# Kernel tuning notes

Hardware: AMD Instinct MI355X
Metric: run time of the kernel (lower is better)

Reference implementation:

```python
import jax, jax.numpy as jnp
import numpy as np

N_NODES = 100000
N_EDGES = 500000
N_REL = 6
IN_DIM = 64
HID = 128
HEADS = 4
C = HID // HEADS  # 32 per-head channels
N_GRAPHS = 1024
EPS = 1e-16


def setup_inputs() -> dict:
    key = jax.random.key(0)
    ks = jax.random.split(key, 20)
    x = jax.random.normal(ks[0], (N_NODES, IN_DIM), dtype=jnp.float32)
    edge_index = jax.random.randint(ks[1], (N_REL, 2, N_EDGES), 0, N_NODES, dtype=jnp.int64)
    batch = jnp.sort(jax.random.randint(ks[2], (N_NODES,), 0, N_GRAPHS, dtype=jnp.int64))
    s = 0.02
    return {
        "x": x, "edge_index": edge_index, "batch": batch,
        # layer1 GAT params (stacked over 6 relations)
        "W1": jax.random.normal(ks[3], (N_REL, IN_DIM, HID), dtype=jnp.float32) * s,
        "as1": jax.random.normal(ks[4], (N_REL, HEADS, C), dtype=jnp.float32) * s,
        "ad1": jax.random.normal(ks[5], (N_REL, HEADS, C), dtype=jnp.float32) * s,
        "b1": jnp.zeros((N_REL, HID), dtype=jnp.float32),
        # layer2 GAT params
        "W2": jax.random.normal(ks[6], (N_REL, HID, HID), dtype=jnp.float32) * s,
        "as2": jax.random.normal(ks[7], (N_REL, HEADS, C), dtype=jnp.float32) * s,
        "ad2": jax.random.normal(ks[8], (N_REL, HEADS, C), dtype=jnp.float32) * s,
        "b2": jnp.zeros((N_REL, HID), dtype=jnp.float32),
        # layernorms
        "g1": jnp.ones((HID,), dtype=jnp.float32), "be1": jnp.zeros((HID,), dtype=jnp.float32),
        "g2": jnp.ones((HID,), dtype=jnp.float32), "be2": jnp.zeros((HID,), dtype=jnp.float32),
        # attention pooling query + output proj
        "q": jax.random.normal(ks[9], (HID,), dtype=jnp.float32) * s,
        "Wp": jax.random.normal(ks[10], (HID, HID), dtype=jnp.float32) * s,
        "bp": jnp.zeros((HID,), dtype=jnp.float32),
    }


def _gat_hetero_layer(x, edge_index, W, a_src, a_dst, b):
    # HeteroConv(aggr='sum') over R GATConv relations, add_self_loops=False, eval (no dropout)
    N = x.shape[0]
    out = jnp.zeros((N, HEADS * C), dtype=x.dtype)
    for r in range(N_REL):
        h = (x @ W[r]).reshape(N, HEADS, C)          # [N,H,C]
        al_s = (h * a_src[r]).sum(-1)                # [N,H]
        al_d = (h * a_dst[r]).sum(-1)                # [N,H]
        src, dst = edge_index[r, 0], edge_index[r, 1]
        e = jax.nn.leaky_relu(al_s[src] + al_d[dst], 0.2)   # [E,H]
        m = jax.ops.segment_max(e, dst, num_segments=N)
        ex = jnp.exp(e - m[dst])
        den = jax.ops.segment_sum(ex, dst, num_segments=N)
        alpha = ex / (den[dst] + EPS)                # segment softmax over incoming edges
        msg = h[src] * alpha[:, :, None]             # [E,H,C]
        agg = jax.ops.segment_sum(msg, dst, num_segments=N).reshape(N, HEADS * C)
        out = out + agg + b[r]
    return out


def _layernorm(x, g, b):
    mu = x.mean(-1, keepdims=True)
    v = ((x - mu) ** 2).mean(-1, keepdims=True)
    return (x - mu) * jax.lax.rsqrt(v + 1e-5) * g + b


def _softsign(x):
    return x / (1.0 + jnp.abs(x))


def reference(x, edge_index, batch, W1, as1, ad1, b1, W2, as2, ad2, b2,
              g1, be1, g2, be2, q, Wp, bp):
    h = _gat_hetero_layer(x, edge_index, W1, as1, ad1, b1)
    h = _layernorm(_softsign(h), g1, be1)
    h = _gat_hetero_layer(h, edge_index, W2, as2, ad2, b2)
    h = _layernorm(_softsign(h), g2, be2)
    # attention pooling: segment softmax over batch, then weighted scatter-sum
    scores = (h * q).sum(-1)                                   # [N]
    m = jax.ops.segment_max(scores, batch, num_segments=N_GRAPHS)
    ex = jnp.exp(scores - m[batch])
    den = jax.ops.segment_sum(ex, batch, num_segments=N_GRAPHS)
    w = ex / (den[batch] + EPS)
    pooled = jax.ops.segment_sum(h * w[:, None], batch, num_segments=N_GRAPHS)  # [G,HID]
    return pooled @ Wp + bp
```

## Files before the change

### kernel.cpp

```cpp
#include <hip/hip_runtime.h>
#include <hip/hip_bf16.h>
#include <hip/hip_fp16.h>

#define N_NODES_C 100000
#define N_EDGES_C 500000
#define N_REL_C 6
#define IN_DIM_C 64
#define HID_C 128
#define HEADS_C 4
#define CPH_C 32
#define N_GRAPHS_C 1024
#define NBLK_SCAN 391

typedef _Float16 f16x8 __attribute__((ext_vector_type(8)));
typedef float f32x4 __attribute__((ext_vector_type(4)));

__global__ __launch_bounds__(256) void hist_rank_kernel(const int* __restrict__ ei,
                                                        int* __restrict__ cnt,
                                                        int* __restrict__ rank) {
    int i = blockIdx.x * 256 + threadIdx.x;
    if (i >= N_REL_C * N_EDGES_C) return;
    int r = i / N_EDGES_C;
    int e = i - r * N_EDGES_C;
    int dst = ei[(size_t)r * 2 * N_EDGES_C + N_EDGES_C + e];
    rank[i] = atomicAdd(&cnt[r * N_NODES_C + dst], 1);
}

__global__ __launch_bounds__(256) void scan1_kernel(const int* __restrict__ cnt,
                                                    int* __restrict__ rowptr,
                                                    int* __restrict__ blocksums) {
    int r = blockIdx.y, b = blockIdx.x, t = threadIdx.x;
    int idx = b * 256 + t;
    int v = (idx < N_NODES_C) ? cnt[r * N_NODES_C + idx] : 0;
    int orig = v;
    int lane = t & 63, w = t >> 6;
#pragma unroll
    for (int off = 1; off < 64; off <<= 1) {
        int n = __shfl_up(v, off);
        if (lane >= off) v += n;
    }
    __shared__ int wt[4];
    if (lane == 63) wt[w] = v;
    __syncthreads();
    int add = 0;
    for (int i = 0; i < w; i++) add += wt[i];
    v += add;
    if (idx < N_NODES_C) rowptr[(size_t)r * (N_NODES_C + 1) + idx] = v - orig;
    if (t == 255) blocksums[r * NBLK_SCAN + b] = v;
}

__global__ __launch_bounds__(512) void scan2_kernel(int* __restrict__ blocksums) {
    int r = blockIdx.x, t = threadIdx.x;
    int v = (t < NBLK_SCAN) ? blocksums[r * NBLK_SCAN + t] : 0;
    int orig = v;
    int lane = t & 63, w = t >> 6;
#pragma unroll
    for (int off = 1; off < 64; off <<= 1) {
        int n = __shfl_up(v, off);
        if (lane >= off) v += n;
    }
    __shared__ int wt[8];
    if (lane == 63) wt[w] = v;
    __syncthreads();
    int add = 0;
    for (int i = 0; i < w; i++) add += wt[i];
    v += add;
    if (t < NBLK_SCAN) blocksums[r * NBLK_SCAN + t] = v - orig;
}

__global__ __launch_bounds__(256) void scatter_kernel(const int* __restrict__ ei,
                                                      const int* __restrict__ rowptrP,
                                                      const int* __restrict__ bsums,
                                                      const int* __restrict__ rank,
                                                      int* __restrict__ srcids) {
    int i = blockIdx.x * 256 + threadIdx.x;
    if (i >= N_REL_C * N_EDGES_C) return;
    int r = i / N_EDGES_C;
    int e = i - r * N_EDGES_C;
    int src = ei[(size_t)r * 2 * N_EDGES_C + e];
    int dst = ei[(size_t)r * 2 * N_EDGES_C + N_EDGES_C + e];
    int base = rowptrP[(size_t)r * (N_NODES_C + 1) + dst] + bsums[r * NBLK_SCAN + (dst >> 8)];
    srcids[(size_t)r * N_EDGES_C + base + rank[i]] = src;
}

__global__ __launch_bounds__(256) void convert_all_kernel(const float* __restrict__ x,
                                                          __half* __restrict__ xh,
                                                          const float* __restrict__ W1,
                                                          const float* __restrict__ W2,
                                                          __half* __restrict__ Wt1,
                                                          __half* __restrict__ Wt2) {
    int i = blockIdx.x * 256 + threadIdx.x;
    if (i < N_NODES_C * IN_DIM_C / 4) {
        float4 v = ((const float4*)x)[i];
        union { __half h[4]; uint2 u; } u;
        u.h[0] = __float2half(v.x); u.h[1] = __float2half(v.y);
        u.h[2] = __float2half(v.z); u.h[3] = __float2half(v.w);
        ((uint2*)xh)[i] = u.u;
    }
    if (i < N_REL_C * IN_DIM_C * HID_C) {
        int r = i / (IN_DIM_C * HID_C);
        int rem = i - r * (IN_DIM_C * HID_C);
        int k = rem / HID_C, n = rem - k * HID_C;
        Wt1[(size_t)r * HID_C * IN_DIM_C + n * IN_DIM_C + k] = __float2half(W1[i]);
    }
    if (i < N_REL_C * HID_C * HID_C) {
        int r = i / (HID_C * HID_C);
        int rem = i - r * (HID_C * HID_C);
        int k = rem / HID_C, n = rem - k * HID_C;
        Wt2[(size_t)r * HID_C * HID_C + n * HID_C + k] = __float2half(W2[i]);
    }
}

template <int K>
__global__ __launch_bounds__(256) void gemm_mfma_kernel(
    const __half* __restrict__ Xh, const __half* __restrict__ Wtbase,
    __half* __restrict__ Hbase, int rel_start, int rel_cnt,
    const float* __restrict__ asbase, const float* __restrict__ adbase,
    float* __restrict__ alsbase, float* __restrict__ aldbase) {
    __shared__ _Float16 sh[4][16][HID_C];
    const int wave = threadIdx.x >> 6, lane = threadIdx.x & 63;
    const int r0 = blockIdx.x * 64 + wave * 16;
    const int m = lane & 15, quad = lane >> 4;
    int arow = r0 + m;
    if (arow > N_NODES_C - 1) arow = N_NODES_C - 1;

    f16x8 afrag[K / 32];
#pragma unroll
    for (int kc = 0; kc < K; kc += 32)
        afrag[kc / 32] = *(const f16x8*)(Xh + (size_t)arow * K + quad * 8 + kc);

    for (int j = 0; j < rel_cnt; j++) {
        int slot = rel_start + j;
        const __half* Wt = Wtbase + (size_t)slot * HID_C * K;
        __half* H = Hbase + (size_t)j * N_NODES_C * HID_C;
        const __half* bp = Wt + (size_t)m * K + quad * 8;

        f32x4 acc[8];
#pragma unroll
        for (int t = 0; t < 8; t++) acc[t] = (f32x4){0.f, 0.f, 0.f, 0.f};
#pragma unroll
        for (int kc = 0; kc < K; kc += 32) {
#pragma unroll
            for (int t = 0; t < 8; t++) {
                f16x8 b = *(const f16x8*)(bp + (size_t)t * 16 * K + kc);
                acc[t] = __builtin_amdgcn_mfma_f32_16x16x32_f16(afrag[kc / 32], b, acc[t], 0, 0, 0);
            }
        }

#pragma unroll
        for (int t = 0; t < 8; t++)
#pragma unroll
            for (int i = 0; i < 4; i++)
                sh[wave][quad * 4 + i][t * 16 + m] = (_Float16)acc[t][i];
#pragma unroll
        for (int p = 0; p < 4; p++) {
            int idx = p * 512 + lane * 8;
            int row = idx >> 7;
            int col = idx & 127;
            int R = r0 + row;
            if (R < N_NODES_C)
                *(uint4*)(H + (size_t)R * HID_C + col) = *(const uint4*)&sh[wave][row][col];
        }

        const float* a_s = asbase + slot * HID_C;
        const float* a_d = adbase + slot * HID_C;
        float* als = alsbase + (size_t)j * N_NODES_C * HEADS_C;
        float* ald = aldbase + (size_t)j * N_NODES_C * HEADS_C;
        float ps[4][4], pd[4][4];
#pragma unroll
        for (int h = 0; h < 4; h++) {
            float as0 = a_s[h * 32 + m], as1 = a_s[h * 32 + 16 + m];
            float ad0 = a_d[h * 32 + m], ad1 = a_d[h * 32 + 16 + m];
#pragma unroll
            for (int i = 0; i < 4; i++) {
                ps[h][i] = acc[2 * h][i] * as0 + acc[2 * h + 1][i] * as1;
                pd[h][i] = acc[2 * h][i] * ad0 + acc[2 * h + 1][i] * ad1;
            }
        }
#pragma unroll
        for (int off = 1; off < 16; off <<= 1) {
#pragma unroll
            for (int h = 0; h < 4; h++)
#pragma unroll
                for (int i = 0; i < 4; i++) {
                    ps[h][i] += __shfl_xor(ps[h][i], off);
                    pd[h][i] += __shfl_xor(pd[h][i], off);
                }
        }
#pragma unroll
        for (int h = 0; h < 4; h++) {
            if (m == h) {
#pragma unroll
                for (int i = 0; i < 4; i++) {
                    int R = r0 + quad * 4 + i;
                    if (R < N_NODES_C) {
                        als[R * HEADS_C + h] = ps[h][i];
                        ald[R * HEADS_C + h] = pd[h][i];
                    }
                }
            }
        }
    }
}

__global__ __launch_bounds__(256) void csr_agg_kernel(
    const int* __restrict__ rowptrP, const int* __restrict__ bsums,
    const int* __restrict__ srcids,
    const __half* __restrict__ A, const float* __restrict__ als,
    const float* __restrict__ ald, int rel_start, int rel_cnt,
    const float* __restrict__ bias, int first, int last,
    float* __restrict__ B,
    const float* __restrict__ g, const float* __restrict__ be,
    __half* __restrict__ Cbh) {
    int node = blockIdx.x * 4 + (threadIdx.x >> 6);
    int lane = threadIdx.x & 63;
    int grp = lane >> 4;
    int j16 = lane & 15;
    int head = j16 >> 2;
    int cbase = j16 * 8;

    float acc[8];
    if (first) {
#pragma unroll
        for (int t = 0; t < 8; t++) {
            float s = 0.f;
#pragma unroll
            for (int r = 0; r < N_REL_C; r++) s += bias[r * HID_C + cbase + t];
            acc[t] = s;
        }
    } else {
        float4 b0 = *(const float4*)(B + (size_t)node * HID_C + cbase);
        float4 b1 = *(const float4*)(B + (size_t)node * HID_C + cbase + 4);
        acc[0] = b0.x; acc[1] = b0.y; acc[2] = b0.z; acc[3] = b0.w;
        acc[4] = b1.x; acc[5] = b1.y; acc[6] = b1.z; acc[7] = b1.w;
    }

    for (int j = 0; j < rel_cnt; j++) {
        int r = rel_start + j;
        const int* rp = rowptrP + (size_t)r * (N_NODES_C + 1);
        const int* bs = bsums + r * NBLK_SCAN;
        const int* sp = srcids + (size_t)r * N_EDGES_C;
        const __half* Aj = A + (size_t)j * N_NODES_C * HID_C;
        const float* alj = als + (size_t)j * N_NODES_C * HEADS_C;
        float aldv = ald[(size_t)j * N_NODES_C * HEADS_C + node * HEADS_C + head];
        int s = rp[node] + bs[node >> 8];
        int e = (node == N_NODES_C - 1) ? N_EDGES_C
                                        : rp[node + 1] + bs[(node + 1) >> 8];
        float racc[8];
#pragma unroll
        for (int t = 0; t < 8; t++) racc[t] = 0.f;
        float rden = 0.f;

        union HU { uint4 u; _Float16 h[8]; };
        int i = s + grp;
        int src = (i < e) ? sp[i] : 0;
        HU rw; rw.u = *(const uint4*)(Aj + (size_t)src * HID_C + cbase);
        float lg = alj[src * HEADS_C + head];
        for (; i < e; i += 4) {
            int nsrc = (i + 4 < e) ? sp[i + 4] : 0;
            HU nrw; nrw.u = *(const uint4*)(Aj + (size_t)nsrc * HID_C + cbase);
            float nlg = alj[nsrc * HEADS_C + head];
            float v = lg + aldv;
            v = fmaxf(v, 0.2f * v);
            float ex = __expf(v);
            rden += ex;
#pragma unroll
            for (int t = 0; t < 8; t++)
                racc[t] = fmaf((float)rw.h[t], ex, racc[t]);
            src = nsrc; rw = nrw; lg = nlg;
        }
#pragma unroll
        for (int off = 16; off < 64; off <<= 1) {
            rden += __shfl_xor(rden, off);
#pragma unroll
            for (int t = 0; t < 8; t++) racc[t] += __shfl_xor(racc[t], off);
        }
        float inv = 1.f / (rden + 1e-16f);
#pragma unroll
        for (int t = 0; t < 8; t++) acc[t] = fmaf(racc[t], inv, acc[t]);
    }

    if (!last) {
        if (grp == 0) {
            float4 o0 = make_float4(acc[0], acc[1], acc[2], acc[3]);
            float4 o1 = make_float4(acc[4], acc[5], acc[6], acc[7]);
            *(float4*)(B + (size_t)node * HID_C + cbase) = o0;
            *(float4*)(B + (size_t)node * HID_C + cbase + 4) = o1;
        }
    } else {
        float ss[8];
        float sum = 0.f, sq = 0.f;
#pragma unroll
        for (int t = 0; t < 8; t++) {
            float v = acc[t] / (1.f + fabsf(acc[t]));
            ss[t] = v;
            sum += v;
            sq = fmaf(v, v, sq);
        }
#pragma unroll
        for (int off = 1; off < 16; off <<= 1) {
            sum += __shfl_xor(sum, off);
            sq += __shfl_xor(sq, off);
        }
        float mu = sum * (1.f / 128.f);
        float var = sq * (1.f / 128.f) - mu * mu;
        float inv = rsqrtf(var + 1e-5f);
        if (grp == 0) {
            float4 gv0 = *(const float4*)(g + cbase);
            float4 gv1 = *(const float4*)(g + cbase + 4);
            float4 bv0 = *(const float4*)(be + cbase);
            float4 bv1 = *(const float4*)(be + cbase + 4);
            union { uint4 u; __half2 h2[4]; } ow;
            ow.h2[0] = __float22half2_rn(make_float2(
                (ss[0] - mu) * inv * gv0.x + bv0.x, (ss[1] - mu) * inv * gv0.y + bv0.y));
            ow.h2[1] = __float22half2_rn(make_float2(
                (ss[2] - mu) * inv * gv0.z + bv0.z, (ss[3] - mu) * inv * gv0.w + bv0.w));
            ow.h2[2] = __float22half2_rn(make_float2(
                (ss[4] - mu) * inv * gv1.x + bv1.x, (ss[5] - mu) * inv * gv1.y + bv1.y));
            ow.h2[3] = __float22half2_rn(make_float2(
                (ss[6] - mu) * inv * gv1.z + bv1.z, (ss[7] - mu) * inv * gv1.w + bv1.w));
            *(uint4*)(Cbh + (size_t)node * HID_C + cbase) = ow.u;
        }
    }
}

__device__ __forceinline__ int lower_bound_i(const int* __restrict__ a, int n, int v) {
    int lo = 0, hi = n;
    while (lo < hi) {
        int mid = (lo + hi) >> 1;
        if (a[mid] < v) lo = mid + 1; else hi = mid;
    }
    return lo;
}

__global__ __launch_bounds__(256) void pool_kernel(const __half* __restrict__ H,
                                                   const int* __restrict__ batch,
                                                   const float* __restrict__ q,
                                                   float* __restrict__ pooled) {
    int g = blockIdx.x;
    int t = threadIdx.x;
    int wave = t >> 6, lane = t & 63;
    int start = lower_bound_i(batch, N_NODES_C, g);
    int end = lower_bound_i(batch, N_NODES_C, g + 1);
    float q0 = q[lane * 2], q1 = q[lane * 2 + 1];
    float p0 = 0.f, p1 = 0.f, den = 0.f;
    for (int n = start + wave; n < end; n += 4) {
        float2 hv = __half22float2(*(const __half2*)(H + (size_t)n * HID_C + lane * 2));
        float part = hv.x * q0 + hv.y * q1;
#pragma unroll
        for (int off = 1; off < 64; off <<= 1) part += __shfl_xor(part, off);
        float exs = __expf(part);
        den += exs;
        p0 = fmaf(exs, hv.x, p0);
        p1 = fmaf(exs, hv.y, p1);
    }
    __shared__ float sp[4][HID_C];
    __shared__ float sden[4];
    sp[wave][lane * 2] = p0;
    sp[wave][lane * 2 + 1] = p1;
    if (lane == 0) sden[wave] = den;
    __syncthreads();
    if (wave == 0) {
        float a0 = sp[0][lane * 2] + sp[1][lane * 2] + sp[2][lane * 2] + sp[3][lane * 2];
        float a1 = sp[0][lane * 2 + 1] + sp[1][lane * 2 + 1] + sp[2][lane * 2 + 1] + sp[3][lane * 2 + 1];
        float d = sden[0] + sden[1] + sden[2] + sden[3];
        float w = 1.f / (d + 1e-16f);
        pooled[(size_t)g * HID_C + lane * 2] = a0 * w;
        pooled[(size_t)g * HID_C + lane * 2 + 1] = a1 * w;
    }
}

__global__ __launch_bounds__(128) void proj_kernel(const float* __restrict__ pooled,
                                                   const float* __restrict__ Wp,
                                                   const float* __restrict__ bp,
                                                   float* __restrict__ out) {
    int g = blockIdx.x, c = threadIdx.x;
    __shared__ float pl[HID_C];
    pl[c] = pooled[(size_t)g * HID_C + c];
    __syncthreads();
    float s = bp[c];
    for (int k = 0; k < HID_C; k++) s = fmaf(pl[k], Wp[k * HID_C + c], s);
    out[(size_t)g * HID_C + c] = s;
}

extern "C" void kernel_launch(void* const* d_in, const int* in_sizes, int n_in,
                              void* d_out, int out_size, void* d_ws, size_t ws_size,
                              hipStream_t stream) {
    const float* x   = (const float*)d_in[0];
    const int* ei    = (const int*)d_in[1];
    const int* batch = (const int*)d_in[2];
    const float* W1  = (const float*)d_in[3];
    const float* as1 = (const float*)d_in[4];
    const float* ad1 = (const float*)d_in[5];
    const float* b1  = (const float*)d_in[6];
    const float* W2  = (const float*)d_in[7];
    const float* as2 = (const float*)d_in[8];
    const float* ad2 = (const float*)d_in[9];
    const float* b2  = (const float*)d_in[10];
    const float* g1  = (const float*)d_in[11];
    const float* be1 = (const float*)d_in[12];
    const float* g2  = (const float*)d_in[13];
    const float* be2 = (const float*)d_in[14];
    const float* q   = (const float*)d_in[15];
    const float* Wp  = (const float*)d_in[16];
    const float* bp  = (const float*)d_in[17];
    float* out = (float*)d_out;

    const size_t NH = (size_t)N_NODES_C * HID_C;
    char* w = (char*)d_ws;
    __half* xh    = (__half*)w;   w += (size_t)N_NODES_C * IN_DIM_C * 2;
    __half* Cbh   = (__half*)w;   w += NH * 2;
    __half* Wt1   = (__half*)w;   w += (size_t)N_REL_C * IN_DIM_C * HID_C * 2;
    __half* Wt2   = (__half*)w;   w += (size_t)N_REL_C * HID_C * HID_C * 2;
    float* pooled = (float*)w;    w += (size_t)N_GRAPHS_C * HID_C * 4;
    int* rowptr   = (int*)w;      w += ((size_t)N_REL_C * (N_NODES_C + 1) * 4 + 15) & ~15ull;
    int* srcids   = (int*)w;      w += (size_t)N_REL_C * N_EDGES_C * 4;
    int* cnt      = (int*)w;      w += (size_t)N_REL_C * N_NODES_C * 4;
    int* bsums    = (int*)w;      w += ((size_t)N_REL_C * NBLK_SCAN * 4 + 15) & ~15ull;

    const size_t fixed_bytes = (size_t)(w - (char*)d_ws);
    const size_t slot_bytes = NH * 2 + 2 * (size_t)N_NODES_C * HEADS_C * 4;
    int nA = 1;
    float* B = nullptr;
    {
        size_t rem = (ws_size > fixed_bytes) ? (ws_size - fixed_bytes) : 0;
        size_t k = rem / slot_bytes;
        if (k >= 6) {
            nA = 6;
        } else {
            size_t rem2 = (rem > NH * 4) ? (rem - NH * 4) : 0;
            size_t k2 = rem2 / slot_bytes;
            nA = (int)(k2 < 1 ? 1 : (k2 > 5 ? 5 : k2));
        }
    }
    float* als = (float*)w;
    float* ald = als + (size_t)nA * N_NODES_C * HEADS_C;
    __half* A  = (__half*)(ald + (size_t)nA * N_NODES_C * HEADS_C);
    if (nA < 6) B = (float*)(A + (size_t)nA * NH);
    int* rank = (int*)A;

    hipMemsetAsync(cnt, 0, (size_t)N_REL_C * N_NODES_C * sizeof(int), stream);
    const int ehg = (N_REL_C * N_EDGES_C + 255) / 256;
    hist_rank_kernel<<<ehg, 256, 0, stream>>>(ei, cnt, rank);
    scan1_kernel<<<dim3(NBLK_SCAN, N_REL_C), 256, 0, stream>>>(cnt, rowptr, bsums);
    scan2_kernel<<<N_REL_C, 512, 0, stream>>>(bsums);
    scatter_kernel<<<ehg, 256, 0, stream>>>(ei, rowptr, bsums, rank, srcids);

    convert_all_kernel<<<(N_NODES_C * IN_DIM_C / 4 + 255) / 256, 256, 0, stream>>>(
        x, xh, W1, W2, Wt1, Wt2);

    const int gemm_grid = (N_NODES_C + 63) / 64;
    const int agg_grid = N_NODES_C / 4;

    for (int gs = 0; gs < N_REL_C; gs += nA) {
        int c2 = (N_REL_C - gs) < nA ? (N_REL_C - gs) : nA;
        gemm_mfma_kernel<IN_DIM_C><<<gemm_grid, 256, 0, stream>>>(
            xh, Wt1, A, gs, c2, as1, ad1, als, ald);
        csr_agg_kernel<<<agg_grid, 256, 0, stream>>>(
            rowptr, bsums, srcids, A, als, ald, gs, c2,
            b1, (gs == 0) ? 1 : 0, (gs + c2 == N_REL_C) ? 1 : 0,
            B, g1, be1, Cbh);
    }
    for (int gs = 0; gs < N_REL_C; gs += nA) {
        int c2 = (N_REL_C - gs) < nA ? (N_REL_C - gs) : nA;
        gemm_mfma_kernel<HID_C><<<gemm_grid, 256, 0, stream>>>(
            Cbh, Wt2, A, gs, c2, as2, ad2, als, ald);
        csr_agg_kernel<<<agg_grid, 256, 0, stream>>>(
            rowptr, bsums, srcids, A, als, ald, gs, c2,
            b2, (gs == 0) ? 1 : 0, (gs + c2 == N_REL_C) ? 1 : 0,
            B, g2, be2, Cbh);
    }

    pool_kernel<<<N_GRAPHS_C, 256, 0, stream>>>(Cbh, batch, q, pooled);
    proj_kernel<<<N_GRAPHS_C, 128, 0, stream>>>(pooled, Wp, bp, out);
}
```

Measured before the change: 1.079 ms.

## Parallelize GEMM over relations via grid.y, pad LDS, fuse convert into histogram

The per-block loop over relations in the MFMA GEMM becomes a second grid dimension, so each block computes one relation and there are up to six times as many blocks. The A fragment is now reloaded per block instead of reused across relations. The LDS staging tile gets row padding to reduce bank conflicts. The fp16 conversion kernel is merged into the edge histogram kernel to save a launch. Slot indexing uses blockIdx.y with pointers pre-offset by the group start.

```diff
diff --git a/kernel.cpp b/kernel.cpp
--- a/kernel.cpp
+++ b/kernel.cpp
@@ -11,19 +11,42 @@
 #define CPH_C 32
 #define N_GRAPHS_C 1024
 #define NBLK_SCAN 391
+#define SH_PAD 8
 
 typedef _Float16 f16x8 __attribute__((ext_vector_type(8)));
 typedef float f32x4 __attribute__((ext_vector_type(4)));
 
-__global__ __launch_bounds__(256) void hist_rank_kernel(const int* __restrict__ ei,
-                                                        int* __restrict__ cnt,
-                                                        int* __restrict__ rank) {
+__global__ __launch_bounds__(256) void hist_rank_convert_kernel(
+    const int* __restrict__ ei, int* __restrict__ cnt, int* __restrict__ rank,
+    const float* __restrict__ x, __half* __restrict__ xh,
+    const float* __restrict__ W1, const float* __restrict__ W2,
+    __half* __restrict__ Wt1, __half* __restrict__ Wt2) {
     int i = blockIdx.x * 256 + threadIdx.x;
-    if (i >= N_REL_C * N_EDGES_C) return;
-    int r = i / N_EDGES_C;
-    int e = i - r * N_EDGES_C;
-    int dst = ei[(size_t)r * 2 * N_EDGES_C + N_EDGES_C + e];
-    rank[i] = atomicAdd(&cnt[r * N_NODES_C + dst], 1);
+    if (i < N_NODES_C * IN_DIM_C / 4) {
+        float4 v = ((const float4*)x)[i];
+        union { __half h[4]; uint2 u; } u;
+        u.h[0] = __float2half(v.x); u.h[1] = __float2half(v.y);
+        u.h[2] = __float2half(v.z); u.h[3] = __float2half(v.w);
+        ((uint2*)xh)[i] = u.u;
+    }
+    if (i < N_REL_C * IN_DIM_C * HID_C) {
+        int r = i / (IN_DIM_C * HID_C);
+        int rem = i - r * (IN_DIM_C * HID_C);
+        int k = rem / HID_C, n = rem - k * HID_C;
+        Wt1[(size_t)r * HID_C * IN_DIM_C + n * IN_DIM_C + k] = __float2half(W1[i]);
+    }
+    if (i < N_REL_C * HID_C * HID_C) {
+        int r = i / (HID_C * HID_C);
+        int rem = i - r * (HID_C * HID_C);
+        int k = rem / HID_C, n = rem - k * HID_C;
+        Wt2[(size_t)r * HID_C * HID_C + n * HID_C + k] = __float2half(W2[i]);
+    }
+    if (i < N_REL_C * N_EDGES_C) {
+        int r = i / N_EDGES_C;
+        int e = i - r * N_EDGES_C;
+        int dst = ei[(size_t)r * 2 * N_EDGES_C + N_EDGES_C + e];
+        rank[i] = atomicAdd(&cnt[r * N_NODES_C + dst], 1);
+    }
 }
 
 __global__ __launch_bounds__(256) void scan1_kernel(const int* __restrict__ cnt,
@@ -83,120 +106,87 @@
     srcids[(size_t)r * N_EDGES_C + base + rank[i]] = src;
 }
 
-__global__ __launch_bounds__(256) void convert_all_kernel(const float* __restrict__ x,
-                                                          __half* __restrict__ xh,
-                                                          const float* __restrict__ W1,
-                                                          const float* __restrict__ W2,
-                                                          __half* __restrict__ Wt1,
-                                                          __half* __restrict__ Wt2) {
-    int i = blockIdx.x * 256 + threadIdx.x;
-    if (i < N_NODES_C * IN_DIM_C / 4) {
-        float4 v = ((const float4*)x)[i];
-        union { __half h[4]; uint2 u; } u;
-        u.h[0] = __float2half(v.x); u.h[1] = __float2half(v.y);
-        u.h[2] = __float2half(v.z); u.h[3] = __float2half(v.w);
-        ((uint2*)xh)[i] = u.u;
-    }
-    if (i < N_REL_C * IN_DIM_C * HID_C) {
-        int r = i / (IN_DIM_C * HID_C);
-        int rem = i - r * (IN_DIM_C * HID_C);
-        int k = rem / HID_C, n = rem - k * HID_C;
-        Wt1[(size_t)r * HID_C * IN_DIM_C + n * IN_DIM_C + k] = __float2half(W1[i]);
-    }
-    if (i < N_REL_C * HID_C * HID_C) {
-        int r = i / (HID_C * HID_C);
-        int rem = i - r * (HID_C * HID_C);
-        int k = rem / HID_C, n = rem - k * HID_C;
-        Wt2[(size_t)r * HID_C * HID_C + n * HID_C + k] = __float2half(W2[i]);
-    }
-}
-
 template <int K>
 __global__ __launch_bounds__(256) void gemm_mfma_kernel(
     const __half* __restrict__ Xh, const __half* __restrict__ Wtbase,
-    __half* __restrict__ Hbase, int rel_start, int rel_cnt,
+    __half* __restrict__ Hbase,
     const float* __restrict__ asbase, const float* __restrict__ adbase,
     float* __restrict__ alsbase, float* __restrict__ aldbase) {
-    __shared__ _Float16 sh[4][16][HID_C];
+    __shared__ _Float16 sh[4][16][HID_C + SH_PAD];
+    const int slot = blockIdx.y;
+    const __half* Wt = Wtbase + (size_t)slot * HID_C * K;
+    __half* H = Hbase + (size_t)slot * N_NODES_C * HID_C;
     const int wave = threadIdx.x >> 6, lane = threadIdx.x & 63;
     const int r0 = blockIdx.x * 64 + wave * 16;
     const int m = lane & 15, quad = lane >> 4;
     int arow = r0 + m;
     if (arow > N_NODES_C - 1) arow = N_NODES_C - 1;
-
-    f16x8 afrag[K / 32];
-#pragma unroll
-    for (int kc = 0; kc < K; kc += 32)
-        afrag[kc / 32] = *(const f16x8*)(Xh + (size_t)arow * K + quad * 8 + kc);
-
-    for (int j = 0; j < rel_cnt; j++) {
-        int slot = rel_start + j;
-        const __half* Wt = Wtbase + (size_t)slot * HID_C * K;
-        __half* H = Hbase + (size_t)j * N_NODES_C * HID_C;
-        const __half* bp = Wt + (size_t)m * K + quad * 8;
-
-        f32x4 acc[8];
-#pragma unroll
-        for (int t = 0; t < 8; t++) acc[t] = (f32x4){0.f, 0.f, 0.f, 0.f};
-#pragma unroll
-        for (int kc = 0; kc < K; kc += 32) {
-#pragma unroll
-            for (int t = 0; t < 8; t++) {
-                f16x8 b = *(const f16x8*)(bp + (size_t)t * 16 * K + kc);
-                acc[t] = __builtin_amdgcn_mfma_f32_16x16x32_f16(afrag[kc / 32], b, acc[t], 0, 0, 0);
+    const __half* ap = Xh + (size_t)arow * K + quad * 8;
+    const __half* bp = Wt + (size_t)m * K + quad * 8;
+
+    f32x4 acc[8];
+#pragma unroll
+    for (int t = 0; t < 8; t++) acc[t] = (f32x4){0.f, 0.f, 0.f, 0.f};
+
+#pragma unroll
+    for (int kc = 0; kc < K; kc += 32) {
+        f16x8 a = *(const f16x8*)(ap + kc);
+#pragma unroll
+        for (int t = 0; t < 8; t++) {
+            f16x8 b = *(const f16x8*)(bp + (size_t)t * 16 * K + kc);
+            acc[t] = __builtin_amdgcn_mfma_f32_16x16x32_f16(a, b, acc[t], 0, 0, 0);
+        }
+    }
+
+#pragma unroll
+    for (int t = 0; t < 8; t++)
+#pragma unroll
+        for (int i = 0; i < 4; i++)
+            sh[wave][quad * 4 + i][t * 16 + m] = (_Float16)acc[t][i];
+#pragma unroll
+    for (int p = 0; p < 4; p++) {
+        int idx = p * 512 + lane * 8;
+        int row = idx >> 7;
+        int col = idx & 127;
+        int R = r0 + row;
+        if (R < N_NODES_C)
+            *(uint4*)(H + (size_t)R * HID_C + col) = *(const uint4*)&sh[wave][row][col];
+    }
+
+    const float* a_s = asbase + slot * HID_C;
+    const float* a_d = adbase + slot * HID_C;
+    float* als = alsbase + (size_t)slot * N_NODES_C * HEADS_C;
+    float* ald = aldbase + (size_t)slot * N_NODES_C * HEADS_C;
+    float ps[4][4], pd[4][4];
+#pragma unroll
+    for (int h = 0; h < 4; h++) {
+        float as0 = a_s[h * 32 + m], as1 = a_s[h * 32 + 16 + m];
+        float ad0 = a_d[h * 32 + m], ad1 = a_d[h * 32 + 16 + m];
+#pragma unroll
+        for (int i = 0; i < 4; i++) {
+            ps[h][i] = acc[2 * h][i] * as0 + acc[2 * h + 1][i] * as1;
+            pd[h][i] = acc[2 * h][i] * ad0 + acc[2 * h + 1][i] * ad1;
+        }
+    }
+#pragma unroll
+    for (int off = 1; off < 16; off <<= 1) {
+#pragma unroll
+        for (int h = 0; h < 4; h++)
+#pragma unroll
+            for (int i = 0; i < 4; i++) {
+                ps[h][i] += __shfl_xor(ps[h][i], off);
+                pd[h][i] += __shfl_xor(pd[h][i], off);
             }
-        }
-
-#pragma unroll
-        for (int t = 0; t < 8; t++)
-#pragma unroll
-            for (int i = 0; i < 4; i++)
-                sh[wave][quad * 4 + i][t * 16 + m] = (_Float16)acc[t][i];
-#pragma unroll
-        for (int p = 0; p < 4; p++) {
-            int idx = p * 512 + lane * 8;
-            int row = idx >> 7;
-            int col = idx & 127;
-            int R = r0 + row;
-            if (R < N_NODES_C)
-                *(uint4*)(H + (size_t)R * HID_C + col) = *(const uint4*)&sh[wave][row][col];
-        }
-
-        const float* a_s = asbase + slot * HID_C;
-        const float* a_d = adbase + slot * HID_C;
-        float* als = alsbase + (size_t)j * N_NODES_C * HEADS_C;
-        float* ald = aldbase + (size_t)j * N_NODES_C * HEADS_C;
-        float ps[4][4], pd[4][4];
-#pragma unroll
-        for (int h = 0; h < 4; h++) {
-            float as0 = a_s[h * 32 + m], as1 = a_s[h * 32 + 16 + m];
-            float ad0 = a_d[h * 32 + m], ad1 = a_d[h * 32 + 16 + m];
+    }
+#pragma unroll
+    for (int h = 0; h < 4; h++) {
+        if (m == h) {
 #pragma unroll
             for (int i = 0; i < 4; i++) {
-                ps[h][i] = acc[2 * h][i] * as0 + acc[2 * h + 1][i] * as1;
-                pd[h][i] = acc[2 * h][i] * ad0 + acc[2 * h + 1][i] * ad1;
-            }
-        }
-#pragma unroll
-        for (int off = 1; off < 16; off <<= 1) {
-#pragma unroll
-            for (int h = 0; h < 4; h++)
-#pragma unroll
-                for (int i = 0; i < 4; i++) {
-                    ps[h][i] += __shfl_xor(ps[h][i], off);
-                    pd[h][i] += __shfl_xor(pd[h][i], off);
-                }
-        }
-#pragma unroll
-        for (int h = 0; h < 4; h++) {
-            if (m == h) {
-#pragma unroll
-                for (int i = 0; i < 4; i++) {
-                    int R = r0 + quad * 4 + i;
-                    if (R < N_NODES_C) {
-                        als[R * HEADS_C + h] = ps[h][i];
-                        ald[R * HEADS_C + h] = pd[h][i];
-                    }
+                int R = r0 + quad * 4 + i;
+                if (R < N_NODES_C) {
+                    als[R * HEADS_C + h] = ps[h][i];
+                    ald[R * HEADS_C + h] = pd[h][i];
                 }
             }
         }
@@ -441,21 +431,19 @@
 
     hipMemsetAsync(cnt, 0, (size_t)N_REL_C * N_NODES_C * sizeof(int), stream);
     const int ehg = (N_REL_C * N_EDGES_C + 255) / 256;
-    hist_rank_kernel<<<ehg, 256, 0, stream>>>(ei, cnt, rank);
+    hist_rank_convert_kernel<<<ehg, 256, 0, stream>>>(ei, cnt, rank, x, xh, W1, W2, Wt1, Wt2);
     scan1_kernel<<<dim3(NBLK_SCAN, N_REL_C), 256, 0, stream>>>(cnt, rowptr, bsums);
     scan2_kernel<<<N_REL_C, 512, 0, stream>>>(bsums);
     scatter_kernel<<<ehg, 256, 0, stream>>>(ei, rowptr, bsums, rank, srcids);
 
-    convert_all_kernel<<<(N_NODES_C * IN_DIM_C / 4 + 255) / 256, 256, 0, stream>>>(
-        x, xh, W1, W2, Wt1, Wt2);
-
     const int gemm_grid = (N_NODES_C + 63) / 64;
     const int agg_grid = N_NODES_C / 4;
 
     for (int gs = 0; gs < N_REL_C; gs += nA) {
         int c2 = (N_REL_C - gs) < nA ? (N_REL_C - gs) : nA;
-        gemm_mfma_kernel<IN_DIM_C><<<gemm_grid, 256, 0, stream>>>(
-            xh, Wt1, A, gs, c2, as1, ad1, als, ald);
+        gemm_mfma_kernel<IN_DIM_C><<<dim3(gemm_grid, c2), 256, 0, stream>>>(
+            xh, Wt1 + (size_t)gs * IN_DIM_C * HID_C, A,
+            as1 + gs * HID_C, ad1 + gs * HID_C, als, ald);
         csr_agg_kernel<<<agg_grid, 256, 0, stream>>>(
             rowptr, bsums, srcids, A, als, ald, gs, c2,
             b1, (gs == 0) ? 1 : 0, (gs + c2 == N_REL_C) ? 1 : 0,
@@ -463,8 +451,9 @@
     }
     for (int gs = 0; gs < N_REL_C; gs += nA) {
         int c2 = (N_REL_C - gs) < nA ? (N_REL_C - gs) : nA;
-        gemm_mfma_kernel<HID_C><<<gemm_grid, 256, 0, stream>>>(
-            Cbh, Wt2, A, gs, c2, as2, ad2, als, ald);
+        gemm_mfma_kernel<HID_C><<<dim3(gemm_grid, c2), 256, 0, stream>>>(
+            Cbh, Wt2 + (size_t)gs * HID_C * HID_C, A,
+            as2 + gs * HID_C, ad2 + gs * HID_C, als, ald);
         csr_agg_kernel<<<agg_grid, 256, 0, stream>>>(
             rowptr, bsums, srcids, A, als, ald, gs, c2,
             b2, (gs == 0) ? 1 : 0, (gs + c2 == N_REL_C) ? 1 : 0,
```

Measured after the change: 1.043 ms (median of 2 runs). 3.3% less time.
